# Performance work log

Hardware: AMD Instinct MI355X
Metric: run time of the kernel (lower is better)

## Reference

```python
import jax, jax.numpy as jnp
import numpy as np

N_NODES = 100000


def spmm(edge_src, edge_dst, edge_val, x):
    """z[dst] += val * x[src] over all edges (COO sparse-dense matmul)."""
    gathered = edge_val[:, None] * x[edge_src]  # [E, d]
    return jax.ops.segment_sum(gathered, edge_dst, num_segments=N_NODES)


def setup_inputs() -> dict:
    key = jax.random.key(0)
    k1, k2, k3, k4, k5, k6 = jax.random.split(key, 6)
    N, E, IN, H, C = N_NODES, 1600000, 256, 128, 40
    features = jax.random.normal(k1, (N, IN), dtype=jnp.float32)
    # xavier_uniform-like init
    b1 = float(np.sqrt(6.0 / (IN + H)))
    b2 = float(np.sqrt(6.0 / (H + C)))
    W1 = jax.random.uniform(k2, (IN, H), dtype=jnp.float32, minval=-b1, maxval=b1)
    W2 = jax.random.uniform(k3, (H, C), dtype=jnp.float32, minval=-b2, maxval=b2)
    edge_src = jax.random.randint(k4, (E,), 0, N, dtype=jnp.int32)
    edge_dst = jnp.sort(jax.random.randint(k5, (E,), 0, N, dtype=jnp.int32))
    # normalized-adjacency-like positive edge weights
    edge_val = jax.random.uniform(k6, (E,), dtype=jnp.float32)
    return {"features": features, "W1": W1, "W2": W2,
            "edge_src": edge_src, "edge_dst": edge_dst, "edge_val": edge_val}


def reference(features, W1, W2, edge_src, edge_dst, edge_val):
    # Decoupled GCN: all dense NN layers first (relu between, none after last) ...
    h = jax.nn.relu(features @ W1)
    h = h @ W2  # [N, num_classes]
    # ... then nlayers (=2) rounds of graph propagation (spmm aggregation)
    h = spmm(edge_src, edge_dst, edge_val, h)
    h = spmm(edge_src, edge_dst, edge_val, h)
    return h
```

## Files before the change

kernel.cpp:

```cpp
#include <hip/hip_runtime.h>
#include <cstddef>
#include <cstdint>

#define IN_DIM 256
#define H_DIM  128
#define C_DIM  40
#define BM     128
#define BK     64
#define LDT    72
#define LDH    136
#define PAD_C  40
#define W2_ROWS 64

typedef short bf16x8 __attribute__((ext_vector_type(8)));
typedef float f32x16 __attribute__((ext_vector_type(16)));
typedef uint  u32x4  __attribute__((ext_vector_type(4)));

__device__ __forceinline__ ushort f2bf(float f) {
  uint u = __builtin_bit_cast(uint, f);
  u += 0x7fffu + ((u >> 16) & 1u);
  return (ushort)(u >> 16);
}
__device__ __forceinline__ float bf2f(uint s) {
  uint u = s << 16;
  return __builtin_bit_cast(float, u);
}
__device__ __forceinline__ uint pack2bf(float a, float b) {
#if __has_builtin(__builtin_amdgcn_cvt_pk_bf16_f32)
  typedef __bf16 bf16v2 __attribute__((ext_vector_type(2)));
  bf16v2 r = __builtin_amdgcn_cvt_pk_bf16_f32(a, b);
  return __builtin_bit_cast(uint, r);
#else
  return (uint)f2bf(a) | ((uint)f2bf(b) << 16);
#endif
}

__global__ void build_row_ptr_kernel(const int* __restrict__ dst, int E,
                                     int* __restrict__ row_ptr, int n1) {
  int n = blockIdx.x * blockDim.x + threadIdx.x;
  if (n >= n1) return;
  int lo = 0, hi = E;
  while (lo < hi) {
    int mid = (lo + hi) >> 1;
    if (dst[mid] < n) lo = mid + 1; else hi = mid;
  }
  row_ptr[n] = lo;
}

__global__ void convert_weights_kernel(const float* __restrict__ W1,
                                       const float* __restrict__ W2,
                                       ushort* __restrict__ w1t,
                                       ushort* __restrict__ w2t) {
  int tid = blockIdx.x * blockDim.x + threadIdx.x;
  if (tid < IN_DIM * H_DIM) {
    int k = tid >> 7, n = tid & 127;
    w1t[n * IN_DIM + k] = f2bf(W1[tid]);
  } else {
    int i = tid - IN_DIM * H_DIM;
    int n = i >> 7, k = i & 127;
    w2t[i] = (n < C_DIM) ? f2bf(W2[k * C_DIM + n]) : (ushort)0;
  }
}

__global__ __launch_bounds__(256, 3) void fused_dense_kernel(
    const float* __restrict__ feat, const ushort* __restrict__ w1t,
    const ushort* __restrict__ w2t, ushort* __restrict__ z0, int N) {
  __shared__ __align__(16) ushort smem[26112];

  const int t = threadIdx.x;
  const int w = t >> 6, l = t & 63;
  const int nb = blockIdx.x * BM;

  f32x16 acc[4];
#pragma unroll
  for (int tn = 0; tn < 4; ++tn)
#pragma unroll
    for (int r = 0; r < 16; ++r) acc[tn][r] = 0.f;

  const int srow = t >> 1;
  const int skh  = (t & 1) << 5;
  int grow = nb + srow; if (grow >= N) grow = N - 1;
  const float*  fp = feat + (size_t)grow * IN_DIM + skh;
  const ushort* wp = w1t + (srow << 8) + skh;

  const ushort* Abase = smem + (w * 32 + (l & 31)) * LDT + ((l >> 5) << 3);
  const ushort* Bbase = smem + 128 * LDT + (l & 31) * LDT + ((l >> 5) << 3);

  for (int kc = 0; kc < IN_DIM; kc += BK) {
    const float4* f4 = (const float4*)(fp + kc);
    uint4* adst = (uint4*)(smem + srow * LDT + skh);
#pragma unroll
    for (int i = 0; i < 4; ++i) {
      float4 v0 = f4[2 * i], v1 = f4[2 * i + 1];
      uint4 pk;
      pk.x = pack2bf(v0.x, v0.y);
      pk.y = pack2bf(v0.z, v0.w);
      pk.z = pack2bf(v1.x, v1.y);
      pk.w = pack2bf(v1.z, v1.w);
      adst[i] = pk;
    }
    const uint4* bsrc = (const uint4*)(wp + kc);
    uint4* bdst = (uint4*)(smem + 128 * LDT + srow * LDT + skh);
#pragma unroll
    for (int i = 0; i < 4; ++i) bdst[i] = bsrc[i];
    __syncthreads();

#pragma unroll
    for (int ks = 0; ks < 4; ++ks) {
      bf16x8 af = *(const bf16x8*)(Abase + ks * 16);
#pragma unroll
      for (int tn = 0; tn < 4; ++tn) {
        bf16x8 bfr = *(const bf16x8*)(Bbase + tn * 32 * LDT + ks * 16);
        acc[tn] = __builtin_amdgcn_mfma_f32_32x32x16_bf16(af, bfr, acc[tn], 0, 0, 0);
      }
    }
    __syncthreads();
  }

#pragma unroll
  for (int tn = 0; tn < 4; ++tn) {
    int col = tn * 32 + (l & 31);
#pragma unroll
    for (int r = 0; r < 16; ++r) {
      int nodeLoc = (r & 3) + 8 * (r >> 2) + 4 * (l >> 5) + 32 * w;
      float v = acc[tn][r];
      smem[nodeLoc * LDH + col] = f2bf(v > 0.f ? v : 0.f);
    }
  }
  {
    int row = t >> 2, c4 = (t & 3) << 5;
    const uint4* src = (const uint4*)(w2t + row * H_DIM + c4);
    uint4* dst = (uint4*)(smem + 128 * LDH + row * LDH + c4);
    dst[0] = src[0];
    dst[1] = src[1];
    dst[2] = src[2];
    dst[3] = src[3];
  }
  __syncthreads();

  f32x16 acc2[2];
#pragma unroll
  for (int tn = 0; tn < 2; ++tn)
#pragma unroll
    for (int r = 0; r < 16; ++r) acc2[tn][r] = 0.f;

  const ushort* Hbase  = smem + (w * 32 + (l & 31)) * LDH + ((l >> 5) << 3);
  const ushort* W2base = smem + 128 * LDH + (l & 31) * LDH + ((l >> 5) << 3);
#pragma unroll
  for (int kb = 0; kb < 8; ++kb) {
    bf16x8 af = *(const bf16x8*)(Hbase + kb * 16);
#pragma unroll
    for (int tn = 0; tn < 2; ++tn) {
      bf16x8 bfr = *(const bf16x8*)(W2base + tn * 32 * LDH + kb * 16);
      acc2[tn] = __builtin_amdgcn_mfma_f32_32x32x16_bf16(af, bfr, acc2[tn], 0, 0, 0);
    }
  }

#pragma unroll
  for (int tn = 0; tn < 2; ++tn) {
    int col = tn * 32 + (l & 31);
    if (col < C_DIM) {
#pragma unroll
      for (int r = 0; r < 16; ++r) {
        int node = nb + 32 * w + (r & 3) + 8 * (r >> 2) + 4 * (l >> 5);
        if (node < N) z0[(size_t)node * PAD_C + col] = f2bf(acc2[tn][r]);
      }
    }
  }
}

__global__ __launch_bounds__(256) void spmm_kernel(
    const int* __restrict__ row_ptr, const int* __restrict__ esrc,
    const float* __restrict__ eval, const ushort* __restrict__ x,
    ushort* __restrict__ zb, float* __restrict__ zf, int N, int out_f32) {
  int node = (blockIdx.x << 2) + (threadIdx.x >> 6);
  if (node >= N) return;
  const int lane = threadIdx.x & 63;
  const int h = lane >> 3;
  const int j = lane & 7;
  const bool act = (j < 5);

  int e   = row_ptr[node];
  int end = row_ptr[node + 1];

  float acc[8];
#pragma unroll
  for (int c = 0; c < 8; ++c) acc[c] = 0.f;

  for (; e + 16 <= end; e += 16) {
    int   s0 = esrc[e + h];
    int   s1 = esrc[e + 8 + h];
    float v0 = eval[e + h];
    float v1 = eval[e + 8 + h];
    if (act) {
      u32x4 a = *(const u32x4*)(x + (size_t)s0 * PAD_C + j * 8);
      u32x4 b = *(const u32x4*)(x + (size_t)s1 * PAD_C + j * 8);
      acc[0] = fmaf(v0, bf2f(a.x & 0xffffu), acc[0]);
      acc[1] = fmaf(v0, bf2f(a.x >> 16),     acc[1]);
      acc[2] = fmaf(v0, bf2f(a.y & 0xffffu), acc[2]);
      acc[3] = fmaf(v0, bf2f(a.y >> 16),     acc[3]);
      acc[4] = fmaf(v0, bf2f(a.z & 0xffffu), acc[4]);
      acc[5] = fmaf(v0, bf2f(a.z >> 16),     acc[5]);
      acc[6] = fmaf(v0, bf2f(a.w & 0xffffu), acc[6]);
      acc[7] = fmaf(v0, bf2f(a.w >> 16),     acc[7]);
      acc[0] = fmaf(v1, bf2f(b.x & 0xffffu), acc[0]);
      acc[1] = fmaf(v1, bf2f(b.x >> 16),     acc[1]);
      acc[2] = fmaf(v1, bf2f(b.y & 0xffffu), acc[2]);
      acc[3] = fmaf(v1, bf2f(b.y >> 16),     acc[3]);
      acc[4] = fmaf(v1, bf2f(b.z & 0xffffu), acc[4]);
      acc[5] = fmaf(v1, bf2f(b.z >> 16),     acc[5]);
      acc[6] = fmaf(v1, bf2f(b.w & 0xffffu), acc[6]);
      acc[7] = fmaf(v1, bf2f(b.w >> 16),     acc[7]);
    }
  }
  for (; e + 8 <= end; e += 8) {
    int   s = esrc[e + h];
    float v = eval[e + h];
    if (act) {
      u32x4 u = *(const u32x4*)(x + (size_t)s * PAD_C + j * 8);
      acc[0] = fmaf(v, bf2f(u.x & 0xffffu), acc[0]);
      acc[1] = fmaf(v, bf2f(u.x >> 16),     acc[1]);
      acc[2] = fmaf(v, bf2f(u.y & 0xffffu), acc[2]);
      acc[3] = fmaf(v, bf2f(u.y >> 16),     acc[3]);
      acc[4] = fmaf(v, bf2f(u.z & 0xffffu), acc[4]);
      acc[5] = fmaf(v, bf2f(u.z >> 16),     acc[5]);
      acc[6] = fmaf(v, bf2f(u.w & 0xffffu), acc[6]);
      acc[7] = fmaf(v, bf2f(u.w >> 16),     acc[7]);
    }
  }
  if (e < end) {
    int ei = e + h;
    int ec = ei < end ? ei : end - 1;
    int   s  = esrc[ec];
    float v0 = eval[ec];
    float v  = ei < end ? v0 : 0.f;
    if (act) {
      u32x4 u = *(const u32x4*)(x + (size_t)s * PAD_C + j * 8);
      acc[0] = fmaf(v, bf2f(u.x & 0xffffu), acc[0]);
      acc[1] = fmaf(v, bf2f(u.x >> 16),     acc[1]);
      acc[2] = fmaf(v, bf2f(u.y & 0xffffu), acc[2]);
      acc[3] = fmaf(v, bf2f(u.y >> 16),     acc[3]);
      acc[4] = fmaf(v, bf2f(u.z & 0xffffu), acc[4]);
      acc[5] = fmaf(v, bf2f(u.z >> 16),     acc[5]);
      acc[6] = fmaf(v, bf2f(u.w & 0xffffu), acc[6]);
      acc[7] = fmaf(v, bf2f(u.w >> 16),     acc[7]);
    }
  }

#pragma unroll
  for (int c = 0; c < 8; ++c) acc[c] += __shfl_xor(acc[c], 8);
#pragma unroll
  for (int c = 0; c < 8; ++c) acc[c] += __shfl_xor(acc[c], 16);
#pragma unroll
  for (int c = 0; c < 8; ++c) acc[c] += __shfl_xor(acc[c], 32);

  if (out_f32) {
    if (lane < 5) {
      float4 o0 = {acc[0], acc[1], acc[2], acc[3]};
      float4 o1 = {acc[4], acc[5], acc[6], acc[7]};
      float* p = zf + (size_t)node * C_DIM + j * 8;
      *(float4*)(p + 0) = o0;
      *(float4*)(p + 4) = o1;
    }
  } else {
    if (lane < 5) {
      uint4 p;
      p.x = (uint)f2bf(acc[0]) | ((uint)f2bf(acc[1]) << 16);
      p.y = (uint)f2bf(acc[2]) | ((uint)f2bf(acc[3]) << 16);
      p.z = (uint)f2bf(acc[4]) | ((uint)f2bf(acc[5]) << 16);
      p.w = (uint)f2bf(acc[6]) | ((uint)f2bf(acc[7]) << 16);
      *(uint4*)(zb + (size_t)node * PAD_C + j * 8) = p;
    }
  }
}

extern "C" void kernel_launch(void* const* d_in, const int* in_sizes, int n_in,
                              void* d_out, int out_size, void* d_ws, size_t ws_size,
                              hipStream_t stream) {
  const float* feat  = (const float*)d_in[0];
  const float* W1    = (const float*)d_in[1];
  const float* W2    = (const float*)d_in[2];
  const int*   esrc  = (const int*)d_in[3];
  const int*   edst  = (const int*)d_in[4];
  const float* evalp = (const float*)d_in[5];
  float* out = (float*)d_out;

  const int N = in_sizes[0] / IN_DIM;
  const int E = in_sizes[3];

  char* ws = (char*)d_ws;
  ushort* z0  = (ushort*)ws;
  ushort* z1  = (ushort*)(ws + (size_t)N * PAD_C * 2);
  ushort* w1t = (ushort*)(ws + (size_t)N * PAD_C * 4);
  ushort* w2t = w1t + IN_DIM * H_DIM;
  int* row_ptr = (int*)((char*)(w2t + W2_ROWS * H_DIM));

  build_row_ptr_kernel<<<(N + 256) / 256, 256, 0, stream>>>(edst, E, row_ptr, N + 1);
  convert_weights_kernel<<<(IN_DIM * H_DIM + W2_ROWS * H_DIM) / 256, 256, 0, stream>>>(
      W1, W2, w1t, w2t);
  fused_dense_kernel<<<(N + BM - 1) / BM, 256, 0, stream>>>(feat, w1t, w2t, z0, N);
  spmm_kernel<<<(N + 3) / 4, 256, 0, stream>>>(row_ptr, esrc, evalp, z0, z1, nullptr, N, 0);
  spmm_kernel<<<(N + 3) / 4, 256, 0, stream>>>(row_ptr, esrc, evalp, z1, nullptr, out, N, 1);
}
```

Baseline: 275.6 us.

## Load GEMM operands directly into MFMA registers and merge setup kernels

The first dense GEMM no longer stages feature and W1 tiles through shared memory. Each lane now loads its MFMA fragments straight from global memory, with a two-deep register double buffer, which removes the LDS writes and the __syncthreads barriers. Separately, the row-pointer build and the weight conversion are merged into one setup kernel to save a launch. The trade-off is that B fragments of W1 are read per wave with less reuse and the A reads become strided per lane, which relies on the cache for efficiency.

```diff
diff --git a/kernel.cpp b/kernel.cpp
--- a/kernel.cpp
+++ b/kernel.cpp
@@ -6,8 +6,6 @@
 #define H_DIM  128
 #define C_DIM  40
 #define BM     128
-#define BK     64
-#define LDT    72
 #define LDH    136
 #define PAD_C  40
 #define W2_ROWS 64
@@ -35,30 +33,28 @@
 #endif
 }
 
-__global__ void build_row_ptr_kernel(const int* __restrict__ dst, int E,
-                                     int* __restrict__ row_ptr, int n1) {
-  int n = blockIdx.x * blockDim.x + threadIdx.x;
-  if (n >= n1) return;
-  int lo = 0, hi = E;
-  while (lo < hi) {
-    int mid = (lo + hi) >> 1;
-    if (dst[mid] < n) lo = mid + 1; else hi = mid;
-  }
-  row_ptr[n] = lo;
-}
-
-__global__ void convert_weights_kernel(const float* __restrict__ W1,
-                                       const float* __restrict__ W2,
-                                       ushort* __restrict__ w1t,
-                                       ushort* __restrict__ w2t) {
+__global__ void setup_kernel(const int* __restrict__ dst, int E,
+                             int* __restrict__ row_ptr, int n1,
+                             const float* __restrict__ W1,
+                             const float* __restrict__ W2,
+                             ushort* __restrict__ w1t,
+                             ushort* __restrict__ w2t) {
   int tid = blockIdx.x * blockDim.x + threadIdx.x;
   if (tid < IN_DIM * H_DIM) {
     int k = tid >> 7, n = tid & 127;
     w1t[n * IN_DIM + k] = f2bf(W1[tid]);
-  } else {
+  } else if (tid < IN_DIM * H_DIM + W2_ROWS * H_DIM) {
     int i = tid - IN_DIM * H_DIM;
     int n = i >> 7, k = i & 127;
     w2t[i] = (n < C_DIM) ? f2bf(W2[k * C_DIM + n]) : (ushort)0;
+  }
+  if (tid < n1) {
+    int lo = 0, hi = E;
+    while (lo < hi) {
+      int mid = (lo + hi) >> 1;
+      if (dst[mid] < tid) lo = mid + 1; else hi = mid;
+    }
+    row_ptr[tid] = lo;
   }
 }
 
@@ -77,44 +73,41 @@
 #pragma unroll
     for (int r = 0; r < 16; ++r) acc[tn][r] = 0.f;
 
-  const int srow = t >> 1;
-  const int skh  = (t & 1) << 5;
-  int grow = nb + srow; if (grow >= N) grow = N - 1;
-  const float*  fp = feat + (size_t)grow * IN_DIM + skh;
-  const ushort* wp = w1t + (srow << 8) + skh;
-
-  const ushort* Abase = smem + (w * 32 + (l & 31)) * LDT + ((l >> 5) << 3);
-  const ushort* Bbase = smem + 128 * LDT + (l & 31) * LDT + ((l >> 5) << 3);
-
-  for (int kc = 0; kc < IN_DIM; kc += BK) {
-    const float4* f4 = (const float4*)(fp + kc);
-    uint4* adst = (uint4*)(smem + srow * LDT + skh);
-#pragma unroll
-    for (int i = 0; i < 4; ++i) {
-      float4 v0 = f4[2 * i], v1 = f4[2 * i + 1];
-      uint4 pk;
-      pk.x = pack2bf(v0.x, v0.y);
-      pk.y = pack2bf(v0.z, v0.w);
-      pk.z = pack2bf(v1.x, v1.y);
-      pk.w = pack2bf(v1.z, v1.w);
-      adst[i] = pk;
-    }
-    const uint4* bsrc = (const uint4*)(wp + kc);
-    uint4* bdst = (uint4*)(smem + 128 * LDT + srow * LDT + skh);
-#pragma unroll
-    for (int i = 0; i < 4; ++i) bdst[i] = bsrc[i];
-    __syncthreads();
-
-#pragma unroll
-    for (int ks = 0; ks < 4; ++ks) {
-      bf16x8 af = *(const bf16x8*)(Abase + ks * 16);
-#pragma unroll
-      for (int tn = 0; tn < 4; ++tn) {
-        bf16x8 bfr = *(const bf16x8*)(Bbase + tn * 32 * LDT + ks * 16);
-        acc[tn] = __builtin_amdgcn_mfma_f32_32x32x16_bf16(af, bfr, acc[tn], 0, 0, 0);
-      }
-    }
-    __syncthreads();
+  int rowA = nb + 32 * w + (l & 31);
+  if (rowA >= N) rowA = N - 1;
+  const float*  ap = feat + (size_t)rowA * IN_DIM + ((l >> 5) << 3);
+  const ushort* bp = w1t + ((l & 31) << 8) + ((l >> 5) << 3);
+
+  float4 Ax[2][2];
+  bf16x8 Bx[2][4];
+
+#pragma unroll
+  for (int ks = 0; ks < 16; ++ks) {
+    const int c = ks & 1;
+    if (ks == 0) {
+      Ax[0][0] = *(const float4*)(ap + 0);
+      Ax[0][1] = *(const float4*)(ap + 4);
+#pragma unroll
+      for (int tn = 0; tn < 4; ++tn)
+        Bx[0][tn] = *(const bf16x8*)(bp + tn * (32 * IN_DIM));
+    }
+    if (ks < 15) {
+      const int n16 = (ks + 1) * 16;
+      Ax[c ^ 1][0] = *(const float4*)(ap + n16);
+      Ax[c ^ 1][1] = *(const float4*)(ap + n16 + 4);
+#pragma unroll
+      for (int tn = 0; tn < 4; ++tn)
+        Bx[c ^ 1][tn] = *(const bf16x8*)(bp + tn * (32 * IN_DIM) + n16);
+    }
+    uint4 pk;
+    pk.x = pack2bf(Ax[c][0].x, Ax[c][0].y);
+    pk.y = pack2bf(Ax[c][0].z, Ax[c][0].w);
+    pk.z = pack2bf(Ax[c][1].x, Ax[c][1].y);
+    pk.w = pack2bf(Ax[c][1].z, Ax[c][1].w);
+    bf16x8 af = __builtin_bit_cast(bf16x8, pk);
+#pragma unroll
+    for (int tn = 0; tn < 4; ++tn)
+      acc[tn] = __builtin_amdgcn_mfma_f32_32x32x16_bf16(af, Bx[c][tn], acc[tn], 0, 0, 0);
   }
 
 #pragma unroll
@@ -295,9 +288,8 @@
   ushort* w2t = w1t + IN_DIM * H_DIM;
   int* row_ptr = (int*)((char*)(w2t + W2_ROWS * H_DIM));
 
-  build_row_ptr_kernel<<<(N + 256) / 256, 256, 0, stream>>>(edst, E, row_ptr, N + 1);
-  convert_weights_kernel<<<(IN_DIM * H_DIM + W2_ROWS * H_DIM) / 256, 256, 0, stream>>>(
-      W1, W2, w1t, w2t);
+  setup_kernel<<<(N + 1 + 255) / 256, 256, 0, stream>>>(
+      edst, E, row_ptr, N + 1, W1, W2, w1t, w2t);
   fused_dense_kernel<<<(N + BM - 1) / BM, 256, 0, stream>>>(feat, w1t, w2t, z0, N);
   spmm_kernel<<<(N + 3) / 4, 256, 0, stream>>>(row_ptr, esrc, evalp, z0, z1, nullptr, N, 0);
   spmm_kernel<<<(N + 3) / 4, 256, 0, stream>>>(row_ptr, esrc, evalp, z1, nullptr, out, N, 1);
```

Result: slower. 301.9 us (+9.5%).
